# Kernel tuning notes

Measured on AMD Instinct MI355X. Metric: run time of the kernel, lower is better.

## Reference

```python
import jax, jax.numpy as jnp
import numpy as np

L, H, P = 32768, 256, 256
DT_MIN, DT_MAX = 0.001, 0.1


def setup_inputs() -> dict:
    key = jax.random.key(0)
    ks = jax.random.split(key, 7)
    signal = jax.random.normal(ks[0], (L, H), jnp.float32)
    # stable HiPPO-like init: negative real part, random imaginary part
    lam_re = -(0.1 + 0.4 * jax.random.uniform(ks[1], (P,), jnp.float32))
    lam_im = jax.random.normal(ks[2], (P,), jnp.float32)
    Lambda_ri = jnp.stack([lam_re, lam_im], axis=-1)            # (P, 2)
    B_ri = jax.random.normal(ks[3], (P, H, 2), jnp.float32) / np.float32(np.sqrt(H))
    C_ri = jax.random.normal(ks[4], (H, P, 2), jnp.float32) / np.float32(np.sqrt(P))
    D = jax.random.uniform(ks[5], (H,), jnp.float32)
    log_step = jnp.log(DT_MIN + (DT_MAX - DT_MIN) * jax.random.uniform(ks[6], (P,), jnp.float32))
    return {"signal": signal, "Lambda_ri": Lambda_ri, "B_ri": B_ri,
            "C_ri": C_ri, "D": D, "log_step": log_step}


def reference(signal, Lambda_ri, B_ri, C_ri, D, log_step):
    # --- get_BC_tilde (bcInit='dense'): B stored real (P,H,2) -> complex ---
    Lambda = jax.lax.complex(Lambda_ri[..., 0], Lambda_ri[..., 1])   # (P,)
    B_tilde = jax.lax.complex(B_ri[..., 0], B_ri[..., 1])            # (P, H)
    C_tilde = jax.lax.complex(C_ri[..., 0], C_ri[..., 1])            # (H, P)

    # --- discretize_zoh ---
    step = jnp.exp(log_step)                                          # (P,) step_scale = 1.0
    Lambda_bar = jnp.exp(Lambda * step)                               # (P,) complex
    B_bar = ((Lambda_bar - 1.0) / Lambda)[:, None] * B_tilde          # (P, H) complex

    # --- apply_ssm: Bu_elements = vmap(u -> B_bar @ u) over time ---
    Bu = signal.astype(Lambda_bar.dtype) @ B_bar.T                    # (L, P) complex
    Lam = jnp.broadcast_to(Lambda_bar, Bu.shape)                      # (L, P)

    def binop(qi, qj):
        A_i, Bu_i = qi
        A_j, Bu_j = qj
        return (A_j * A_i, Bu_j + A_j * Bu_i)

    _, xs = jax.lax.associative_scan(binop, (Lam, Bu), axis=0)        # (L, P)

    # y = Re(C_tilde @ x) + D * u, vectorized over time
    y = jnp.real(xs @ C_tilde.T) + D * signal                         # (L, H)
    return y
```

## Files before the change

### kernel.cpp

```cpp
#include <hip/hip_runtime.h>
#include <math.h>

constexpr int L = 32768;
constexpr int H = 256;
constexpr int P = 256;
constexpr int T = 64;
constexpr int NC = L / T;
constexpr int N1 = 2 * P;
constexpr int LDA = 40;
constexpr int LDEP = 130;

typedef __attribute__((ext_vector_type(8))) short short8;
typedef __attribute__((ext_vector_type(4))) float f32x4;

__device__ __forceinline__ unsigned f2bf(float f) {
  unsigned u = __float_as_uint(f);
  return (u + 0x7FFFu + ((u >> 16) & 1u)) >> 16;
}
__device__ __forceinline__ float bf_lo(unsigned u) { return __uint_as_float(u << 16); }
__device__ __forceinline__ float bf_hi(unsigned u) { return __uint_as_float(u & 0xFFFF0000u); }

__device__ __forceinline__ void gload_lds16(const unsigned short* g, unsigned short* l) {
  __builtin_amdgcn_global_load_lds(
      (const __attribute__((address_space(1))) unsigned int*)(g),
      (__attribute__((address_space(3))) unsigned int*)(l), 16, 0, 0);
}

#define KBAR(N) do { \
    asm volatile("s_waitcnt vmcnt(" #N ") lgkmcnt(0)" ::: "memory"); \
    __builtin_amdgcn_s_barrier(); \
    __builtin_amdgcn_sched_barrier(0); \
  } while (0)

#define VMEM_FENCE() __builtin_amdgcn_sched_barrier(0x38F)

__device__ __forceinline__ void lambda_bar_of(const float* __restrict__ lam,
                                              const float* __restrict__ lstep,
                                              int p, float& lbr, float& lbi) {
  float lr = lam[2 * p], li = lam[2 * p + 1];
  float st = expf(lstep[p]);
  float ea = expf(lr * st);
  lbr = ea * cosf(li * st);
  lbi = ea * sinf(li * st);
}

__global__ __launch_bounds__(256) void k_prep(const float* __restrict__ sig,
                                              const float* __restrict__ lam,
                                              const float* __restrict__ lstep,
                                              const float* __restrict__ Bri,
                                              const float* __restrict__ Cri,
                                              unsigned short* __restrict__ Bcat,
                                              unsigned short* __restrict__ Ccat,
                                              float* __restrict__ powr,
                                              float* __restrict__ powi,
                                              unsigned short* __restrict__ sigt) {
  int idx = blockIdx.x * 256 + threadIdx.x;
  if (idx < N1 * H) {
    int n = idx >> 8, k = idx & 255;
    int p = n >> 1, comp = n & 1;
    float lr = lam[2 * p], li = lam[2 * p + 1];
    float st = expf(lstep[p]);
    float ea = expf(lr * st);
    float lbr = ea * cosf(li * st), lbi = ea * sinf(li * st);
    float inv = 1.0f / (lr * lr + li * li);
    float nr = lbr - 1.0f;
    float fr = (nr * lr + lbi * li) * inv;
    float fi = (lbi * lr - nr * li) * inv;
    float br = Bri[2 * (p * H + k)], bi = Bri[2 * (p * H + k) + 1];
    float v = (comp == 0) ? (fr * br - fi * bi) : (fr * bi + fi * br);
    Bcat[idx] = (unsigned short)f2bf(v);
  } else if (idx < 2 * N1 * H) {
    int j = idx - N1 * H;
    int h = j >> 9, k2 = j & 511;
    int p = k2 >> 1;
    float v = ((k2 & 1) == 0) ? Cri[2 * (h * P + p)] : -Cri[2 * (h * P + p) + 1];
    Ccat[j] = (unsigned short)f2bf(v);
  } else if (idx < 2 * N1 * H + T * P) {
    int r = idx - 2 * N1 * H;
    int t = r >> 8, p = r & 255;
    float lr = lam[2 * p], li = lam[2 * p + 1];
    float st = expf(lstep[p]);
    float e = (float)(t + 1);
    float er = expf(e * lr * st);
    powr[r] = er * cosf(e * li * st);
    powi[r] = er * sinf(e * li * st);
  } else {
    int C = idx - (2 * N1 * H + T * P);
    int panel = C >> 12;
    int ks = (C >> 9) & 7;
    int c = C & 511;
    int row = ((c >> 8) << 6) + (((c >> 6) & 3) << 4) + (c & 15);
    int kk = ((c >> 4) & 3) << 3;
    const float* s = sig + (size_t)(panel * 128 + row) * 256 + ks * 32 + kk;
    float4 a = *(const float4*)(s);
    float4 b = *(const float4*)(s + 4);
    uint4 w;
    w.x = f2bf(a.x) | (f2bf(a.y) << 16);
    w.y = f2bf(a.z) | (f2bf(a.w) << 16);
    w.z = f2bf(b.x) | (f2bf(b.y) << 16);
    w.w = f2bf(b.z) | (f2bf(b.w) << 16);
    *(uint4*)(sigt + (size_t)C * 8) = w;
  }
}

__global__ __launch_bounds__(256, 4) void k_gemm1s(const unsigned short* __restrict__ sigt,
                                                   const unsigned short* __restrict__ Bcat,
                                                   const float* __restrict__ lam,
                                                   const float* __restrict__ lstep,
                                                   unsigned short* __restrict__ Xl,
                                                   float* __restrict__ Sr,
                                                   float* __restrict__ Si) {
  constexpr int NIT = 8;
  __shared__ __align__(16) char smem[40960];
  unsigned short* sA[3] = {(unsigned short*)smem, (unsigned short*)(smem + 8192),
                           (unsigned short*)(smem + 16384)};
  unsigned short* sB[2] = {(unsigned short*)(smem + 24576), (unsigned short*)(smem + 32768)};
  float* sEpi = (float*)smem;
  const int tid = threadIdx.x;
  const int lane = tid & 63;
  const int wave = tid >> 6;
  const int wc = (wave & 1) * 64;
  const int m0 = blockIdx.x * 128, n0 = blockIdx.y * 128;
  const int brow = ((tid >> 6) << 4) | (tid & 15);
  const int bko = ((tid >> 4) & 3) * 8;
  const int hb = (wave & 1) * 2048;
  const int afb = (wave >> 1) * 256;
  const unsigned short* apan = sigt + (size_t)blockIdx.x * 32768;
  f32x4 acc[4][4];
#pragma unroll
  for (int i = 0; i < 4; i++)
#pragma unroll
    for (int j = 0; j < 4; j++) acc[i][j] = (f32x4){0.f, 0.f, 0.f, 0.f};

#define ISSUE_A1(ks, buf) { \
    gload_lds16(apan + (ks) * 4096 + tid * 8, sA[buf] + tid * 8); \
    gload_lds16(apan + (ks) * 4096 + 2048 + tid * 8, sA[buf] + 2048 + tid * 8); }
#define ISSUE_B1(ks, buf) { \
    gload_lds16(Bcat + (size_t)(n0 + brow) * 256 + (ks) * 32 + bko, sB[buf] + tid * 8); \
    gload_lds16(Bcat + (size_t)(n0 + 64 + brow) * 256 + (ks) * 32 + bko, sB[buf] + 2048 + tid * 8); }

  ISSUE_A1(0, 0);
  VMEM_FENCE();
  ISSUE_B1(0, 0);
  VMEM_FENCE();
  ISSUE_A1(1, 1);
  VMEM_FENCE();
  KBAR(2);
#pragma unroll
  for (int it = 0; it < NIT; it++) {
    if (it + 1 < NIT) ISSUE_B1(it + 1, (it + 1) & 1);
    VMEM_FENCE();
    if (it + 2 < NIT) ISSUE_A1(it + 2, (it + 2) % 3);
    VMEM_FENCE();
    const unsigned short* sAc = sA[it % 3];
    const unsigned short* sBc = sB[it & 1];
    short8 af[4], bfr[4];
#pragma unroll
    for (int i = 0; i < 4; i++) af[i] = *(const short8*)(sAc + (afb + i * 64 + lane) * 8);
#pragma unroll
    for (int j = 0; j < 4; j++) bfr[j] = *(const short8*)(sBc + hb + (j * 64 + lane) * 8);
#pragma unroll
    for (int i = 0; i < 4; i++)
#pragma unroll
      for (int j = 0; j < 4; j++)
        acc[i][j] = __builtin_amdgcn_mfma_f32_16x16x32_bf16(af[i], bfr[j], acc[i][j], 0, 0, 0);
    if (it + 1 < NIT) {
      if (it + 2 < NIT) { KBAR(2); } else { KBAR(0); }
    }
  }
  __syncthreads();

  const int crow = (lane >> 4) * 4, ccol = wc + (lane & 15);
#pragma unroll
  for (int half = 0; half < 2; half++) {
    if ((wave >> 1) == half) {
#pragma unroll
      for (int i = 0; i < 4; i++)
#pragma unroll
        for (int j = 0; j < 4; j++)
#pragma unroll
          for (int g = 0; g < 4; g++)
            sEpi[(crow + i * 16 + g) * LDEP + ccol + j * 16] = acc[i][j][g];
    }
    __syncthreads();
    if (tid < 64) {
      const int pl = tid;
      const int gp = (n0 >> 1) + pl;
      const int c = blockIdx.x * 2 + half;
      float lbr, lbi;
      lambda_bar_of(lam, lstep, gp, lbr, lbi);
      float xr = 0.f, xi = 0.f;
      const float* e = sEpi + 2 * pl;
      const size_t gbase = (size_t)(m0 + half * 64) * N1 + n0 + 2 * pl;
      for (int tb = 0; tb < T; tb += 8) {
        float2 v[8];
#pragma unroll
        for (int u = 0; u < 8; u++) v[u] = *(const float2*)(e + (tb + u) * LDEP);
        unsigned ov[8];
#pragma unroll
        for (int u = 0; u < 8; u++) {
          float nr = fmaf(lbr, xr, fmaf(-lbi, xi, v[u].x));
          float ni = fmaf(lbr, xi, fmaf(lbi, xr, v[u].y));
          xr = nr; xi = ni;
          ov[u] = f2bf(xr) | (f2bf(xi) << 16);
        }
#pragma unroll
        for (int u = 0; u < 8; u++)
          *(unsigned*)(Xl + gbase + (size_t)(tb + u) * N1) = ov[u];
      }
      Sr[(size_t)gp * NC + c] = xr;
      Si[(size_t)gp * NC + c] = xi;
    }
    __syncthreads();
  }
#undef ISSUE_A1
#undef ISSUE_B1
}

__global__ __launch_bounds__(64) void k_carry2(const float* __restrict__ lam,
                                               const float* __restrict__ lstep,
                                               const float* __restrict__ Sr,
                                               const float* __restrict__ Si,
                                               float* __restrict__ car, float* __restrict__ cai) {
  const int p = blockIdx.x;
  const int t = threadIdx.x;
  float lr = lam[2 * p], li = lam[2 * p + 1];
  float st = expf(lstep[p]);
  float eT = expf((float)T * lr * st);
  float lTr = eT * cosf((float)T * li * st);
  float lTi = eT * sinf((float)T * li * st);
  float vr[8], vi[8];
  {
    const float* srp = Sr + (size_t)p * NC + t * 8;
    const float* sip = Si + (size_t)p * NC + t * 8;
    float4 a0 = *(const float4*)(srp), a1 = *(const float4*)(srp + 4);
    float4 b0 = *(const float4*)(sip), b1 = *(const float4*)(sip + 4);
    vr[0] = a0.x; vr[1] = a0.y; vr[2] = a0.z; vr[3] = a0.w;
    vr[4] = a1.x; vr[5] = a1.y; vr[6] = a1.z; vr[7] = a1.w;
    vi[0] = b0.x; vi[1] = b0.y; vi[2] = b0.z; vi[3] = b0.w;
    vi[4] = b1.x; vi[5] = b1.y; vi[6] = b1.z; vi[7] = b1.w;
  }
  float Br = 0.f, Bi = 0.f;
#pragma unroll
  for (int u = 0; u < 8; u++) {
    float nr = fmaf(lTr, Br, fmaf(-lTi, Bi, vr[u]));
    float ni = fmaf(lTr, Bi, fmaf(lTi, Br, vi[u]));
    Br = nr; Bi = ni;
  }
  float e8 = expf(8.0f * (float)T * lr * st);
  float Ar = e8 * cosf(8.0f * (float)T * li * st);
  float Ai = e8 * sinf(8.0f * (float)T * li * st);
#pragma unroll
  for (int d = 1; d < 64; d <<= 1) {
    float Aor = __shfl_up(Ar, d), Aoi = __shfl_up(Ai, d);
    float Bor = __shfl_up(Br, d), Boi = __shfl_up(Bi, d);
    if (t >= d) {
      float nBr = Ar * Bor - Ai * Boi + Br;
      float nBi = Ar * Boi + Ai * Bor + Bi;
      float nAr = Aor * Ar - Aoi * Ai;
      float nAi = Aor * Ai + Aoi * Ar;
      Br = nBr; Bi = nBi; Ar = nAr; Ai = nAi;
    }
  }
  float cr = __shfl_up(Br, 1), ci = __shfl_up(Bi, 1);
  if (t == 0) { cr = 0.f; ci = 0.f; }
#pragma unroll
  for (int u = 0; u < 8; u++) {
    car[(t * 8 + u) * P + p] = cr;
    cai[(t * 8 + u) * P + p] = ci;
    float nr = fmaf(lTr, cr, fmaf(-lTi, ci, vr[u]));
    float ni = fmaf(lTr, ci, fmaf(lTi, cr, vi[u]));
    cr = nr; ci = ni;
  }
}

__global__ __launch_bounds__(256, 3) void k_gemm2f(const unsigned short* __restrict__ Xl,
                                                   const unsigned short* __restrict__ Ccat,
                                                   const float* __restrict__ powr,
                                                   const float* __restrict__ powi,
                                                   const float* __restrict__ car,
                                                   const float* __restrict__ cai,
                                                   const float* __restrict__ sig,
                                                   const float* __restrict__ Dv,
                                                   float* __restrict__ out) {
  constexpr int K = 512, NIT = K / 32;
  __shared__ __align__(16) char smem[53248];
  unsigned short* sA[2] = {(unsigned short*)smem, (unsigned short*)smem + 5120};
  unsigned short* sB[4] = {(unsigned short*)(smem + 20480), (unsigned short*)(smem + 28672),
                           (unsigned short*)(smem + 36864), (unsigned short*)(smem + 45056)};
  const int tid = threadIdx.x;
  const int lane = tid & 63;
  const int wave = tid >> 6;
  const int wr = (wave >> 1) * 64, wc = (wave & 1) * 64;
  const int m0 = blockIdx.x * 128, n0 = blockIdx.y * 128;
  const int ar = tid >> 1, aq = (tid & 1) * 16;
  const int t_ = ar & 63;
  const int cc = blockIdx.x * 2 + (ar >> 6);
  const int brow = ((tid >> 6) << 4) | (tid & 15);
  const int bko = ((tid >> 4) & 3) * 8;
  const int frow = lane & 15, fk = (lane >> 4) * 8;
  const int hb = (wave & 1) * 2048;
  f32x4 acc[4][4];
#pragma unroll
  for (int i = 0; i < 4; i++)
#pragma unroll
    for (int j = 0; j < 4; j++) acc[i][j] = (f32x4){0.f, 0.f, 0.f, 0.f};

  uint4 x0a, x1a, x0b, x1b;
  float4 pra0, pra1, pia0, pia1, cra0, cra1, cia0, cia1;
  float4 prb0, prb1, pib0, pib1, crb0, crb1, cib0, cib1;
  const unsigned short* xbase = Xl + (size_t)(m0 + ar) * N1 + aq;
  const float* prb = powr + t_ * P;
  const float* pib = powi + t_ * P;
  const float* crb = car + cc * P;
  const float* cib = cai + cc * P;
#define LOAD_X(A0, A1, k0) { \
    A0 = *(const uint4*)(xbase + (k0)); A1 = *(const uint4*)(xbase + (k0) + 8); }
#define LOAD_PC(PR0, PR1, PI0, PI1, CR0, CR1, CI0, CI1, k0) { \
    const int p0_ = ((k0) >> 1) + (tid & 1) * 8; \
    PR0 = *(const float4*)(prb + p0_); PR1 = *(const float4*)(prb + p0_ + 4); \
    PI0 = *(const float4*)(pib + p0_); PI1 = *(const float4*)(pib + p0_ + 4); \
    CR0 = *(const float4*)(crb + p0_); CR1 = *(const float4*)(crb + p0_ + 4); \
    CI0 = *(const float4*)(cib + p0_); CI1 = *(const float4*)(cib + p0_ + 4); }
#define WRITE_A2(XA, XB, PR0, PR1, PI0, PI1, CR0, CR1, CI0, CI1, dst) { \
    unsigned xw[8] = {XA.x, XA.y, XA.z, XA.w, XB.x, XB.y, XB.z, XB.w}; \
    float pr_[8] = {PR0.x, PR0.y, PR0.z, PR0.w, PR1.x, PR1.y, PR1.z, PR1.w}; \
    float pi_[8] = {PI0.x, PI0.y, PI0.z, PI0.w, PI1.x, PI1.y, PI1.z, PI1.w}; \
    float cr_[8] = {CR0.x, CR0.y, CR0.z, CR0.w, CR1.x, CR1.y, CR1.z, CR1.w}; \
    float ci_[8] = {CI0.x, CI0.y, CI0.z, CI0.w, CI1.x, CI1.y, CI1.z, CI1.w}; \
    unsigned wo[8]; \
    _Pragma("unroll") for (int j_ = 0; j_ < 8; j_++) { \
      float xgr = bf_lo(xw[j_]) + (pr_[j_] * cr_[j_] - pi_[j_] * ci_[j_]); \
      float xgi = bf_hi(xw[j_]) + (pr_[j_] * ci_[j_] + pi_[j_] * cr_[j_]); \
      wo[j_] = f2bf(xgr) | (f2bf(xgi) << 16); } \
    uint4 w0, w1; \
    w0.x = wo[0]; w0.y = wo[1]; w0.z = wo[2]; w0.w = wo[3]; \
    w1.x = wo[4]; w1.y = wo[5]; w1.z = wo[6]; w1.w = wo[7]; \
    *(uint4*)((dst) + ar * LDA + aq) = w0; *(uint4*)((dst) + ar * LDA + aq + 8) = w1; }
#define ISSUE_B2(k0, buf) { \
    gload_lds16(Ccat + (size_t)(n0 + brow) * K + (k0) + bko, sB[buf] + tid * 8); \
    gload_lds16(Ccat + (size_t)(n0 + 64 + brow) * K + (k0) + bko, sB[buf] + 2048 + tid * 8); }

  LOAD_X(x0a, x1a, 0);
  LOAD_PC(pra0, pra1, pia0, pia1, cra0, cra1, cia0, cia1, 0);
  LOAD_X(x0b, x1b, 32);
  LOAD_PC(prb0, prb1, pib0, pib1, crb0, crb1, cib0, cib1, 32);
  VMEM_FENCE();
  ISSUE_B2(0, 0);
  ISSUE_B2(32, 1);
  ISSUE_B2(64, 2);
  VMEM_FENCE();
  WRITE_A2(x0a, x1a, pra0, pra1, pia0, pia1, cra0, cra1, cia0, cia1, sA[0]);
  LOAD_X(x0a, x1a, 64);
  LOAD_PC(pra0, pra1, pia0, pia1, cra0, cra1, cia0, cia1, 64);
  VMEM_FENCE();
  KBAR(14);
#pragma unroll
  for (int it = 0; it < NIT; it++) {
    if (it + 1 < NIT) {
      if (((it + 1) & 1) == 0) {
        WRITE_A2(x0a, x1a, pra0, pra1, pia0, pia1, cra0, cra1, cia0, cia1, sA[0]);
      } else {
        WRITE_A2(x0b, x1b, prb0, prb1, pib0, pib1, crb0, crb1, cib0, cib1, sA[1]);
      }
    }
    VMEM_FENCE();
    if (it + 3 < NIT) {
      if (((it + 3) & 1) == 0) {
        LOAD_X(x0a, x1a, (it + 3) * 32);
        LOAD_PC(pra0, pra1, pia0, pia1, cra0, cra1, cia0, cia1, (it + 3) * 32);
      } else {
        LOAD_X(x0b, x1b, (it + 3) * 32);
        LOAD_PC(prb0, prb1, pib0, pib1, crb0, crb1, cib0, cib1, (it + 3) * 32);
      }
    }
    VMEM_FENCE();
    if (it + 3 < NIT) ISSUE_B2((it + 3) * 32, (it + 3) & 3);
    VMEM_FENCE();
    short8 af[4], bfr[4];
#pragma unroll
    for (int i = 0; i < 4; i++) af[i] = *(const short8*)(sA[it & 1] + (wr + i * 16 + frow) * LDA + fk);
#pragma unroll
    for (int j = 0; j < 4; j++) bfr[j] = *(const short8*)(sB[it & 3] + hb + (j * 64 + lane) * 8);
#pragma unroll
    for (int i = 0; i < 4; i++)
#pragma unroll
      for (int j = 0; j < 4; j++)
        acc[i][j] = __builtin_amdgcn_mfma_f32_16x16x32_bf16(af[i], bfr[j], acc[i][j], 0, 0, 0);
    if (it + 1 < NIT) {
      if (it < NIT - 3) { KBAR(24); }
      else if (it == NIT - 3) { KBAR(12); }
      else { KBAR(0); }
    }
  }

  const int crow = wr + (lane >> 4) * 4, ccol = wc + (lane & 15);
  float dcol[4];
#pragma unroll
  for (int j = 0; j < 4; j++) dcol[j] = Dv[n0 + ccol + j * 16];
#pragma unroll
  for (int i = 0; i < 4; i++)
#pragma unroll
    for (int j = 0; j < 4; j++) {
      int col = n0 + ccol + j * 16;
#pragma unroll
      for (int g = 0; g < 4; g++) {
        int row = m0 + crow + i * 16 + g;
        out[(size_t)row * H + col] = acc[i][j][g] + dcol[j] * sig[(size_t)row * H + col];
      }
    }
#undef LOAD_X
#undef LOAD_PC
#undef WRITE_A2
#undef ISSUE_B2
}

extern "C" void kernel_launch(void* const* d_in, const int* in_sizes, int n_in,
                              void* d_out, int out_size, void* d_ws, size_t ws_size,
                              hipStream_t stream) {
  const float* sig = (const float*)d_in[0];
  const float* lam = (const float*)d_in[1];
  const float* Bri = (const float*)d_in[2];
  const float* Cri = (const float*)d_in[3];
  const float* Dv  = (const float*)d_in[4];
  const float* lst = (const float*)d_in[5];
  float* out = (float*)d_out;

  unsigned short* Bcat = (unsigned short*)d_ws;
  unsigned short* Ccat = Bcat + (size_t)N1 * H;
  unsigned short* Xl   = Ccat + (size_t)H * N1;
  float* powr = (float*)(Xl + (size_t)L * N1);
  float* powi = powr + T * P;
  float* Sr   = powi + T * P;
  float* Si   = Sr + NC * P;
  float* car  = Si + NC * P;
  float* cai  = car + NC * P;
  unsigned short* sigt = (unsigned short*)(cai + NC * P);

  k_prep<<<(2 * N1 * H + T * P + L * H / 8) / 256, 256, 0, stream>>>(
      sig, lam, lst, Bri, Cri, Bcat, Ccat, powr, powi, sigt);
  dim3 g1(L / 128, N1 / 128);
  k_gemm1s<<<g1, 256, 0, stream>>>(sigt, Bcat, lam, lst, Xl, Sr, Si);
  k_carry2<<<NC / 2, 64, 0, stream>>>(lam, lst, Sr, Si, car, cai);
  dim3 g2(L / 128, H / 128);
  k_gemm2f<<<g2, 256, 0, stream>>>(Xl, Ccat, powr, powi, car, cai, sig, Dv, out);
}
```

Before: 152.4 us.

## Split carry fix-up into separate kernel writing MFMA-ready panels for GEMM2

The carry correction (X + pow*carry) that was fused into the second GEMM's A-tile load now runs in a new k_fix kernel. That kernel writes a bf16 buffer already laid out in the MFMA fragment order, so the GEMM can stream A straight into LDS with direct global-to-LDS loads. The GEMM tile changes from 128x128 to 128x64, with triple-buffered A, double-buffered B, less shared memory and higher occupancy. The cost is an extra launch and an extra write and read of the 32 MB intermediate, plus the A panel is now read twice because there are more column blocks.

After: 156.5 us. 2.7% more time.

```diff
diff --git a/kernel.cpp b/kernel.cpp
--- a/kernel.cpp
+++ b/kernel.cpp
@@ -7,7 +7,6 @@
 constexpr int T = 64;
 constexpr int NC = L / T;
 constexpr int N1 = 2 * P;
-constexpr int LDA = 40;
 constexpr int LDEP = 130;
 
 typedef __attribute__((ext_vector_type(8))) short short8;
@@ -274,134 +273,121 @@
   }
 }
 
-__global__ __launch_bounds__(256, 3) void k_gemm2f(const unsigned short* __restrict__ Xl,
+__device__ __forceinline__ unsigned mix1(unsigned u, float pr, float pi, float cr, float ci) {
+  float re = bf_lo(u) + (pr * cr - pi * ci);
+  float im = bf_hi(u) + (pr * ci + pi * cr);
+  return f2bf(re) | (f2bf(im) << 16);
+}
+
+__global__ __launch_bounds__(256) void k_fix(const unsigned short* __restrict__ Xl,
+                                             const float* __restrict__ powr,
+                                             const float* __restrict__ powi,
+                                             const float* __restrict__ car,
+                                             const float* __restrict__ cai,
+                                             unsigned short* __restrict__ Xg) {
+  int g = blockIdx.x * 256 + threadIdx.x;
+  int row = g >> 4, seg = g & 15;
+  int t = row & 63, cidx = row >> 6, rowp = row & 127, panel = row >> 7;
+  int p0 = seg * 16;
+  const unsigned short* xs = Xl + (size_t)row * N1 + seg * 32;
+  uint4 x0 = *(const uint4*)(xs);
+  uint4 x1 = *(const uint4*)(xs + 8);
+  uint4 x2 = *(const uint4*)(xs + 16);
+  uint4 x3 = *(const uint4*)(xs + 24);
+  const float* prB = powr + t * P + p0;
+  const float* piB = powi + t * P + p0;
+  const float* crB = car + cidx * P + p0;
+  const float* ciB = cai + cidx * P + p0;
+  const int cb = ((rowp >> 6) << 8) | (((rowp >> 4) & 3) << 6) | (rowp & 15);
+  unsigned short* xd = Xg + (size_t)panel * 65536 + (size_t)seg * 4096 + cb * 8;
+#define FIXQ(XQ, q) { \
+    float4 pr = *(const float4*)(prB + 4 * (q)); \
+    float4 pi = *(const float4*)(piB + 4 * (q)); \
+    float4 cr = *(const float4*)(crB + 4 * (q)); \
+    float4 ci = *(const float4*)(ciB + 4 * (q)); \
+    uint4 o; \
+    o.x = mix1(XQ.x, pr.x, pi.x, cr.x, ci.x); \
+    o.y = mix1(XQ.y, pr.y, pi.y, cr.y, ci.y); \
+    o.z = mix1(XQ.z, pr.z, pi.z, cr.z, ci.z); \
+    o.w = mix1(XQ.w, pr.w, pi.w, cr.w, ci.w); \
+    *(uint4*)(xd + (q) * 128) = o; }
+  FIXQ(x0, 0);
+  FIXQ(x1, 1);
+  FIXQ(x2, 2);
+  FIXQ(x3, 3);
+#undef FIXQ
+}
+
+__global__ __launch_bounds__(256, 4) void k_gemm2p(const unsigned short* __restrict__ Xg,
                                                    const unsigned short* __restrict__ Ccat,
-                                                   const float* __restrict__ powr,
-                                                   const float* __restrict__ powi,
-                                                   const float* __restrict__ car,
-                                                   const float* __restrict__ cai,
                                                    const float* __restrict__ sig,
                                                    const float* __restrict__ Dv,
                                                    float* __restrict__ out) {
-  constexpr int K = 512, NIT = K / 32;
-  __shared__ __align__(16) char smem[53248];
-  unsigned short* sA[2] = {(unsigned short*)smem, (unsigned short*)smem + 5120};
-  unsigned short* sB[4] = {(unsigned short*)(smem + 20480), (unsigned short*)(smem + 28672),
-                           (unsigned short*)(smem + 36864), (unsigned short*)(smem + 45056)};
+  constexpr int NIT = 16;
+  __shared__ __align__(16) char smem[32768];
+  unsigned short* sA[3] = {(unsigned short*)smem, (unsigned short*)(smem + 8192),
+                           (unsigned short*)(smem + 16384)};
+  unsigned short* sB[2] = {(unsigned short*)(smem + 24576), (unsigned short*)(smem + 28672)};
   const int tid = threadIdx.x;
   const int lane = tid & 63;
   const int wave = tid >> 6;
-  const int wr = (wave >> 1) * 64, wc = (wave & 1) * 64;
-  const int m0 = blockIdx.x * 128, n0 = blockIdx.y * 128;
-  const int ar = tid >> 1, aq = (tid & 1) * 16;
-  const int t_ = ar & 63;
-  const int cc = blockIdx.x * 2 + (ar >> 6);
-  const int brow = ((tid >> 6) << 4) | (tid & 15);
+  const int m0 = blockIdx.x * 128, n0 = blockIdx.y * 64;
+  const int brow = (((tid >> 6) & 3) << 4) | (tid & 15);
   const int bko = ((tid >> 4) & 3) * 8;
-  const int frow = lane & 15, fk = (lane >> 4) * 8;
-  const int hb = (wave & 1) * 2048;
-  f32x4 acc[4][4];
+  const int afb = (wave >> 1) * 256;
+  const int bfb = (wave & 1) * 2;
+  const unsigned short* apan = Xg + (size_t)blockIdx.x * 65536;
+  f32x4 acc[4][2];
 #pragma unroll
   for (int i = 0; i < 4; i++)
 #pragma unroll
-    for (int j = 0; j < 4; j++) acc[i][j] = (f32x4){0.f, 0.f, 0.f, 0.f};
-
-  uint4 x0a, x1a, x0b, x1b;
-  float4 pra0, pra1, pia0, pia1, cra0, cra1, cia0, cia1;
-  float4 prb0, prb1, pib0, pib1, crb0, crb1, cib0, cib1;
-  const unsigned short* xbase = Xl + (size_t)(m0 + ar) * N1 + aq;
-  const float* prb = powr + t_ * P;
-  const float* pib = powi + t_ * P;
-  const float* crb = car + cc * P;
-  const float* cib = cai + cc * P;
-#define LOAD_X(A0, A1, k0) { \
-    A0 = *(const uint4*)(xbase + (k0)); A1 = *(const uint4*)(xbase + (k0) + 8); }
-#define LOAD_PC(PR0, PR1, PI0, PI1, CR0, CR1, CI0, CI1, k0) { \
-    const int p0_ = ((k0) >> 1) + (tid & 1) * 8; \
-    PR0 = *(const float4*)(prb + p0_); PR1 = *(const float4*)(prb + p0_ + 4); \
-    PI0 = *(const float4*)(pib + p0_); PI1 = *(const float4*)(pib + p0_ + 4); \
-    CR0 = *(const float4*)(crb + p0_); CR1 = *(const float4*)(crb + p0_ + 4); \
-    CI0 = *(const float4*)(cib + p0_); CI1 = *(const float4*)(cib + p0_ + 4); }
-#define WRITE_A2(XA, XB, PR0, PR1, PI0, PI1, CR0, CR1, CI0, CI1, dst) { \
-    unsigned xw[8] = {XA.x, XA.y, XA.z, XA.w, XB.x, XB.y, XB.z, XB.w}; \
-    float pr_[8] = {PR0.x, PR0.y, PR0.z, PR0.w, PR1.x, PR1.y, PR1.z, PR1.w}; \
-    float pi_[8] = {PI0.x, PI0.y, PI0.z, PI0.w, PI1.x, PI1.y, PI1.z, PI1.w}; \
-    float cr_[8] = {CR0.x, CR0.y, CR0.z, CR0.w, CR1.x, CR1.y, CR1.z, CR1.w}; \
-    float ci_[8] = {CI0.x, CI0.y, CI0.z, CI0.w, CI1.x, CI1.y, CI1.z, CI1.w}; \
-    unsigned wo[8]; \
-    _Pragma("unroll") for (int j_ = 0; j_ < 8; j_++) { \
-      float xgr = bf_lo(xw[j_]) + (pr_[j_] * cr_[j_] - pi_[j_] * ci_[j_]); \
-      float xgi = bf_hi(xw[j_]) + (pr_[j_] * ci_[j_] + pi_[j_] * cr_[j_]); \
-      wo[j_] = f2bf(xgr) | (f2bf(xgi) << 16); } \
-    uint4 w0, w1; \
-    w0.x = wo[0]; w0.y = wo[1]; w0.z = wo[2]; w0.w = wo[3]; \
-    w1.x = wo[4]; w1.y = wo[5]; w1.z = wo[6]; w1.w = wo[7]; \
-    *(uint4*)((dst) + ar * LDA + aq) = w0; *(uint4*)((dst) + ar * LDA + aq + 8) = w1; }
-#define ISSUE_B2(k0, buf) { \
-    gload_lds16(Ccat + (size_t)(n0 + brow) * K + (k0) + bko, sB[buf] + tid * 8); \
-    gload_lds16(Ccat + (size_t)(n0 + 64 + brow) * K + (k0) + bko, sB[buf] + 2048 + tid * 8); }
-
-  LOAD_X(x0a, x1a, 0);
-  LOAD_PC(pra0, pra1, pia0, pia1, cra0, cra1, cia0, cia1, 0);
-  LOAD_X(x0b, x1b, 32);
-  LOAD_PC(prb0, prb1, pib0, pib1, crb0, crb1, cib0, cib1, 32);
+    for (int j = 0; j < 2; j++) acc[i][j] = (f32x4){0.f, 0.f, 0.f, 0.f};
+
+#define ISSUE_A2(ks, buf) { \
+    gload_lds16(apan + (ks) * 4096 + tid * 8, sA[buf] + tid * 8); \
+    gload_lds16(apan + (ks) * 4096 + 2048 + tid * 8, sA[buf] + 2048 + tid * 8); }
+#define ISSUE_B2(ks, buf) { \
+    gload_lds16(Ccat + (size_t)(n0 + brow) * 512 + (ks) * 32 + bko, sB[buf] + tid * 8); }
+
+  ISSUE_A2(0, 0);
   VMEM_FENCE();
   ISSUE_B2(0, 0);
-  ISSUE_B2(32, 1);
-  ISSUE_B2(64, 2);
-  VMEM_FENCE();
-  WRITE_A2(x0a, x1a, pra0, pra1, pia0, pia1, cra0, cra1, cia0, cia1, sA[0]);
-  LOAD_X(x0a, x1a, 64);
-  LOAD_PC(pra0, pra1, pia0, pia1, cra0, cra1, cia0, cia1, 64);
-  VMEM_FENCE();
-  KBAR(14);
+  VMEM_FENCE();
+  ISSUE_A2(1, 1);
+  VMEM_FENCE();
+  KBAR(2);
 #pragma unroll
   for (int it = 0; it < NIT; it++) {
-    if (it + 1 < NIT) {
-      if (((it + 1) & 1) == 0) {
-        WRITE_A2(x0a, x1a, pra0, pra1, pia0, pia1, cra0, cra1, cia0, cia1, sA[0]);
-      } else {
-        WRITE_A2(x0b, x1b, prb0, prb1, pib0, pib1, crb0, crb1, cib0, cib1, sA[1]);
-      }
-    }
+    if (it + 1 < NIT) ISSUE_B2(it + 1, (it + 1) & 1);
     VMEM_FENCE();
-    if (it + 3 < NIT) {
-      if (((it + 3) & 1) == 0) {
-        LOAD_X(x0a, x1a, (it + 3) * 32);
-        LOAD_PC(pra0, pra1, pia0, pia1, cra0, cra1, cia0, cia1, (it + 3) * 32);
-      } else {
-        LOAD_X(x0b, x1b, (it + 3) * 32);
-        LOAD_PC(prb0, prb1, pib0, pib1, crb0, crb1, cib0, cib1, (it + 3) * 32);
-      }
-    }
+    if (it + 2 < NIT) ISSUE_A2(it + 2, (it + 2) % 3);
     VMEM_FENCE();
-    if (it + 3 < NIT) ISSUE_B2((it + 3) * 32, (it + 3) & 3);
-    VMEM_FENCE();
-    short8 af[4], bfr[4];
-#pragma unroll
-    for (int i = 0; i < 4; i++) af[i] = *(const short8*)(sA[it & 1] + (wr + i * 16 + frow) * LDA + fk);
-#pragma unroll
-    for (int j = 0; j < 4; j++) bfr[j] = *(const short8*)(sB[it & 3] + hb + (j * 64 + lane) * 8);
+    const unsigned short* sAc = sA[it % 3];
+    const unsigned short* sBc = sB[it & 1];
+    short8 af[4], bfr[2];
+#pragma unroll
+    for (int i = 0; i < 4; i++) af[i] = *(const short8*)(sAc + (afb + i * 64 + lane) * 8);
+#pragma unroll
+    for (int j = 0; j < 2; j++) bfr[j] = *(const short8*)(sBc + ((bfb + j) * 64 + lane) * 8);
 #pragma unroll
     for (int i = 0; i < 4; i++)
 #pragma unroll
-      for (int j = 0; j < 4; j++)
+      for (int j = 0; j < 2; j++)
         acc[i][j] = __builtin_amdgcn_mfma_f32_16x16x32_bf16(af[i], bfr[j], acc[i][j], 0, 0, 0);
     if (it + 1 < NIT) {
-      if (it < NIT - 3) { KBAR(24); }
-      else if (it == NIT - 3) { KBAR(12); }
-      else { KBAR(0); }
-    }
-  }
-
-  const int crow = wr + (lane >> 4) * 4, ccol = wc + (lane & 15);
-  float dcol[4];
-#pragma unroll
-  for (int j = 0; j < 4; j++) dcol[j] = Dv[n0 + ccol + j * 16];
+      if (it + 2 < NIT) { KBAR(2); } else { KBAR(0); }
+    }
+  }
+
+  const int crow = (wave >> 1) * 64 + (lane >> 4) * 4;
+  const int ccol = (wave & 1) * 32 + (lane & 15);
+  float dcol[2];
+#pragma unroll
+  for (int j = 0; j < 2; j++) dcol[j] = Dv[n0 + ccol + j * 16];
 #pragma unroll
   for (int i = 0; i < 4; i++)
 #pragma unroll
-    for (int j = 0; j < 4; j++) {
+    for (int j = 0; j < 2; j++) {
       int col = n0 + ccol + j * 16;
 #pragma unroll
       for (int g = 0; g < 4; g++) {
@@ -409,9 +395,7 @@
         out[(size_t)row * H + col] = acc[i][j][g] + dcol[j] * sig[(size_t)row * H + col];
       }
     }
-#undef LOAD_X
-#undef LOAD_PC
-#undef WRITE_A2
+#undef ISSUE_A2
 #undef ISSUE_B2
 }
 
@@ -436,12 +420,14 @@
   float* car  = Si + NC * P;
   float* cai  = car + NC * P;
   unsigned short* sigt = (unsigned short*)(cai + NC * P);
+  unsigned short* Xg   = sigt + (size_t)L * H;
 
   k_prep<<<(2 * N1 * H + T * P + L * H / 8) / 256, 256, 0, stream>>>(
       sig, lam, lst, Bri, Cri, Bcat, Ccat, powr, powi, sigt);
   dim3 g1(L / 128, N1 / 128);
   k_gemm1s<<<g1, 256, 0, stream>>>(sigt, Bcat, lam, lst, Xl, Sr, Si);
   k_carry2<<<NC / 2, 64, 0, stream>>>(lam, lst, Sr, Si, car, cai);
-  dim3 g2(L / 128, H / 128);
-  k_gemm2f<<<g2, 256, 0, stream>>>(Xl, Ccat, powr, powi, car, cai, sig, Dv, out);
-}
+  k_fix<<<L * 16 / 256, 256, 0, stream>>>(Xl, powr, powi, car, cai, Xg);
+  dim3 g2(L / 128, H / 64);
+  k_gemm2p<<<g2, 256, 0, stream>>>(Xg, Ccat, sig, Dv, out);
+}
```
